# Kernel tuning notes

Hardware: AMD Instinct MI355X
Metric: run time of the kernel (lower is better)

The kernel has to match this reference:

```python
import jax, jax.numpy as jnp
import numpy as np

N, C, H, W = 4, 256, 32, 32
NH = 2                      # att_nhead
HD = C // NH                # 128 per-head dim
MAX_DIS = 7
WS = 2 * MAX_DIS + 1        # 15 window side
WW = WS * WS                # 225 window positions
T = (C / NH) ** 0.5


def _gather_idx(h, w):
    # idx[wpos, m]: flat index into zero-padded (h+14, w+14) grid of the
    # neighbor at window offset wpos for query pixel m (== F.unfold semantics)
    pw = w + 2 * MAX_DIS
    dy, dx = np.meshgrid(np.arange(WS), np.arange(WS), indexing='ij')
    ys, xs = np.meshgrid(np.arange(h), np.arange(w), indexing='ij')
    idx = (dy.reshape(-1, 1) + ys.reshape(1, -1)) * pw + (dx.reshape(-1, 1) + xs.reshape(1, -1))
    return jnp.asarray(idx, dtype=jnp.int32)  # [WW, h*w]


def setup_inputs() -> dict:
    key = jax.random.key(0)
    ks = jax.random.split(key, 14)
    s = 0.02
    return {
        'q': jax.random.normal(ks[0], (N, C, H, W), jnp.float32),
        'k': jax.random.normal(ks[1], (N, C, H, W), jnp.float32),
        'v': jax.random.normal(ks[2], (N, C, H, W), jnp.float32),
        'Wq': jax.random.normal(ks[3], (C, C), jnp.float32) * s,
        'bq': jnp.zeros((C,), jnp.float32),
        'Wk': jax.random.normal(ks[4], (C, C), jnp.float32) * s,
        'bk': jnp.zeros((C,), jnp.float32),
        'Wv': jax.random.normal(ks[5], (C, C), jnp.float32) * s,
        'bv': jnp.zeros((C,), jnp.float32),
        'Wrel': jax.random.normal(ks[6], (NH, WW, HD), jnp.float32) * s,   # grouped 1x1 conv
        'brel': jnp.zeros((NH * WW,), jnp.float32),
        'V_bias': jax.random.normal(ks[7], (NH, HD, WW), jnp.float32) * s,
        'Wfc': jax.random.normal(ks[8], (C, C), jnp.float32) * s,
        'bfc': jnp.zeros((C,), jnp.float32),
    }


def _conv1x1(x, Wt, b):
    return jnp.einsum('nchw,dc->ndhw', x, Wt) + b[None, :, None, None]


def reference(q, k, v, Wq, bq, Wk, bk, Wv, bv, Wrel, brel, V_bias, Wfc, bfc):
    n, c, h, w = q.shape
    hw = h * w
    idx = _gather_idx(h, w)                                   # [WW, hw]
    pad = ((0, 0), (0, 0), (0, 0), (MAX_DIS, MAX_DIS), (MAX_DIS, MAX_DIS))

    q = _conv1x1(q, Wq, bq)
    k = _conv1x1(k, Wk, bk)
    v = _conv1x1(v, Wv, bv)

    # grouped 1x1 conv: relative position logits, [n, NH, WW, hw]
    rel = jnp.einsum('ngcxy,gwc->ngwxy', q.reshape(n, NH, HD, h, w), Wrel)
    rel = rel + brel.reshape(NH, WW)[None, :, :, None, None]
    rel = rel.reshape(n, NH, WW, hw)

    qs = (q / T).reshape(n, NH, HD, hw)

    # unfold K via zero-pad + gather: [n, NH, HD, WW, hw]
    k_pad = jnp.pad(k.reshape(n, NH, HD, h, w), pad).reshape(n, NH, HD, -1)
    k_un = k_pad[..., idx]
    qk = jnp.einsum('ngcm,ngcwm->ngwm', qs, k_un) + rel

    # boundary mask: neighbor inside the original image
    valid = jnp.pad(jnp.ones((h, w), jnp.float32), MAX_DIS).reshape(-1)[idx] > 0
    qk = jnp.where(valid[None, None], qk, jnp.float32(-1e8))
    attn = jax.nn.softmax(qk, axis=2)                         # over window positions

    agg_bias = jnp.einsum('ngwm,gcw->mngc', attn, V_bias).reshape(hw, n, c)

    # local2global scatter + dense einsum == gather of zero-padded V
    v_pad = jnp.pad(v.reshape(n, NH, HD, h, w), pad).reshape(n, NH, HD, -1)
    v_un = v_pad[..., idx]                                    # [n, NH, HD, WW, hw]
    agg_value = jnp.einsum('ngwm,ngcwm->mngc', attn, v_un).reshape(hw, n, c)

    out = (agg_value + agg_bias) @ Wfc.T + bfc                # [hw, n, c]
    return out
```

## Files before the change

### kernel.cpp

```cpp
#include <hip/hip_runtime.h>
#include <math.h>


typedef __attribute__((ext_vector_type(8))) short short8;
typedef __attribute__((ext_vector_type(4))) short short4v;
typedef __attribute__((ext_vector_type(4))) float floatx4;

__device__ __forceinline__ short f2bf(float f) {
    unsigned u = __float_as_uint(f);
    unsigned r = (u + 0x7fffu + ((u >> 16) & 1u)) >> 16;
    return (short)r;
}
__device__ __forceinline__ float bf2f(short s) {
    return __uint_as_float(((unsigned)(unsigned short)s) << 16);
}

__global__ __launch_bounds__(256)
void conv_kernel(const float* __restrict__ q, const float* __restrict__ k,
                 const float* __restrict__ v,
                 const float* __restrict__ Wq, const float* __restrict__ Wk,
                 const float* __restrict__ Wv, const float* __restrict__ Wfc,
                 const float* __restrict__ Wrel,
                 short* __restrict__ Xhi, short* __restrict__ Xlo,
                 short* __restrict__ Whi, short* __restrict__ Wlo,
                 short* __restrict__ Wrh, short* __restrict__ Wrl)
{
    const int tid = threadIdx.x;
    const int z = blockIdx.z;
    const int lane = tid & 63;
    const int n16 = lane & 15, quad = lane >> 4;

    if (z < 12) {
        __shared__ float st[64 * 33];
        const int sel = z >> 2, batch = z & 3;
        const float* X = (sel == 0 ? q : sel == 1 ? k : v) + ((long)batch << 18);
        const int mb = blockIdx.x, kc = blockIdx.y;
#pragma unroll
        for (int it = 0; it < 8; ++it) {
            int e = tid + it * 256;
            int cc = e >> 6, mm = e & 63;
            st[mm * 33 + cc] = X[((long)(kc * 32 + cc) << 10) + mb * 64 + mm];
        }
        __syncthreads();
        const int mtl = tid >> 6;
        const int m = mtl * 16 + n16;
        short h[8], l[8];
#pragma unroll
        for (int j = 0; j < 8; ++j) {
            float f = st[m * 33 + quad * 8 + j];
            short hb = f2bf(f);
            h[j] = hb;
            l[j] = f2bf(f - bf2f(hb));
        }
        int mt16 = mb * 4 + mtl;
        long off = (long)z * 262144 + (((long)(mt16 * 8 + kc) * 64) + lane) * 8;
        *(short8*)(Xhi + off) = *(short8*)&h[0];
        *(short8*)(Xlo + off) = *(short8*)&l[0];
    } else if (z < 16) {
        if (tid >= 64) return;
        const int w = z - 12;
        const float* W = (w == 0 ? Wq : w == 1 ? Wk : w == 2 ? Wv : Wfc);
        const int dt = blockIdx.x, kc = blockIdx.y;
        const int d = dt * 16 + n16, cb = kc * 32 + quad * 8;
        float4 w0 = *(const float4*)&W[d * 256 + cb];
        float4 w1 = *(const float4*)&W[d * 256 + cb + 4];
        float f[8] = {w0.x, w0.y, w0.z, w0.w, w1.x, w1.y, w1.z, w1.w};
        short h[8], l[8];
#pragma unroll
        for (int j = 0; j < 8; ++j) {
            short hb = f2bf(f[j]);
            h[j] = hb;
            l[j] = f2bf(f[j] - bf2f(hb));
        }
        long off = (long)w * 65536 + (((long)(dt * 8 + kc) * 64) + lane) * 8;
        *(short8*)(Whi + off) = *(short8*)&h[0];
        *(short8*)(Wlo + off) = *(short8*)&l[0];
    } else {
        if (tid >= 64) return;
        const int g = z - 16;
        const int wt = blockIdx.x, kc = blockIdx.y;
        if (wt >= 15 || kc >= 4) return;
        const int w = wt * 16 + n16;
        const int cb = kc * 32 + quad * 8;
        float f[8] = {0.f, 0.f, 0.f, 0.f, 0.f, 0.f, 0.f, 0.f};
        if (w < 225) {
            float4 w0 = *(const float4*)&Wrel[(long)(g * 225 + w) * 128 + cb];
            float4 w1 = *(const float4*)&Wrel[(long)(g * 225 + w) * 128 + cb + 4];
            f[0] = w0.x; f[1] = w0.y; f[2] = w0.z; f[3] = w0.w;
            f[4] = w1.x; f[5] = w1.y; f[6] = w1.z; f[7] = w1.w;
        }
        short h[8], l[8];
#pragma unroll
        for (int j = 0; j < 8; ++j) {
            short hb = f2bf(f[j]);
            h[j] = hb;
            l[j] = f2bf(f[j] - bf2f(hb));
        }
        long off = (long)g * 30720 + (((long)(wt * 4 + kc) * 64) + lane) * 8;
        *(short8*)(Wrh + off) = *(short8*)&h[0];
        *(short8*)(Wrl + off) = *(short8*)&l[0];
    }
}

__global__ __launch_bounds__(256)
void mfma_proj(const short* __restrict__ Xhi, const short* __restrict__ Xlo,
               const short* __restrict__ Whi, const short* __restrict__ Wlo,
               const float* __restrict__ bq, const float* __restrict__ bk,
               const float* __restrict__ bv,
               short* __restrict__ qhi, short* __restrict__ qlo,
               short* __restrict__ khi, short* __restrict__ klo,
               float* __restrict__ vpad)
{
    __shared__ float tile[16 * 65];
    const int tid = threadIdx.x;
    const int wave = tid >> 6, lane = tid & 63;
    const int n16 = lane & 15, quad = lane >> 4;
    const int mt16 = blockIdx.x, db = blockIdx.y, z = blockIdx.z;
    const int sel = z >> 2, batch = z & 3;
    const int dt = db * 4 + wave;

    const short* Ah = Whi + (long)sel * 65536 + ((long)(dt * 8) * 64 + lane) * 8;
    const short* Al = Wlo + (long)sel * 65536 + ((long)(dt * 8) * 64 + lane) * 8;
    const short* Bh = Xhi + (long)z * 262144;
    const short* Bl = Xlo + (long)z * 262144;

    const float* bias = (sel == 0 ? bq : sel == 1 ? bk : bv);
    float4 bv4 = *(const float4*)&bias[dt * 16 + quad * 4];
    float bb[4] = {bv4.x, bv4.y, bv4.z, bv4.w};

    floatx4 acc = {0.f, 0.f, 0.f, 0.f};
#pragma unroll
    for (int kc = 0; kc < 8; ++kc) {
        short8 ahi = *(const short8*)(Ah + kc * 512);
        short8 alo = *(const short8*)(Al + kc * 512);
        long bo = ((long)(mt16 * 8 + kc) * 64 + lane) * 8;
        short8 bh = *(const short8*)(Bh + bo);
        short8 bl = *(const short8*)(Bl + bo);
        acc = __builtin_amdgcn_mfma_f32_16x16x32_bf16(ahi, bh, acc, 0, 0, 0);
        acc = __builtin_amdgcn_mfma_f32_16x16x32_bf16(ahi, bl, acc, 0, 0, 0);
        acc = __builtin_amdgcn_mfma_f32_16x16x32_bf16(alo, bh, acc, 0, 0, 0);
    }

    if (sel == 2) {
        const int m = mt16 * 16 + n16;
        float* Y = vpad + (long)batch * 393216;
        const int row = m >> 5, col = (m & 31) + 8;
#pragma unroll
        for (int r = 0; r < 4; ++r)
            Y[(long)(dt * 16 + quad * 4 + r) * 1536 + row * 48 + col] = acc[r] + bb[r];
        {
            const int prow = mt16 >> 1, side = mt16 & 1;
            const int ch_l = tid >> 2, f2 = (tid & 3) * 2;
            long po = (long)(db * 64 + ch_l) * 1536 + prow * 48 + side * 40 + f2;
            Y[po] = 0.f;
            Y[po + 1] = 0.f;
        }
        return;
    }

    const int cl = wave * 16 + quad * 4;
#pragma unroll
    for (int r = 0; r < 4; ++r)
        tile[n16 * 65 + cl + r] = acc[r] + bb[r];
    __syncthreads();

    const float scale = (sel == 1) ? 0.08838834764831845f : 1.0f;
    const int m_l = tid >> 4, c16 = (tid & 15) * 4;
    const int m = mt16 * 16 + m_l;
    const int cglob = db * 64 + c16;
    const int g = cglob >> 7, ch = cglob & 127;
    const long base = (((long)(batch * 2 + g) << 10) + m) * 128 + ch;
    short h[4], l[4];
#pragma unroll
    for (int j = 0; j < 4; ++j) {
        float f = tile[m_l * 65 + c16 + j] * scale;
        short hb = f2bf(f);
        h[j] = hb;
        l[j] = f2bf(f - bf2f(hb));
    }
    short* oh = sel ? khi : qhi;
    short* ol = sel ? klo : qlo;
    *(short4v*)(oh + base) = *(short4v*)&h[0];
    *(short4v*)(ol + base) = *(short4v*)&l[0];
}

__global__ __launch_bounds__(256)
void scores_mfma(const short* __restrict__ qhi, const short* __restrict__ qlo,
                 const short* __restrict__ khi, const short* __restrict__ klo,
                 const short* __restrict__ Wrh, const short* __restrict__ Wrl,
                 const float* __restrict__ brel, float* __restrict__ attn)
{
    __shared__ float qk[16 * 241];
    __shared__ float invl[16];

    const int tid = threadIdx.x;
    const int wave = tid >> 6, lane = tid & 63;
    const int y  = blockIdx.x >> 1;
    const int xt = blockIdx.x & 1;
    const int bz = blockIdx.y;
    const int g = bz & 1;
    const int x0 = xt * 16;
    float* relh = attn + (long)bz * 230400;

    const int n16 = lane & 15, quad = lane >> 4;
    const long qbase = (((long)bz << 10) + y * 32 + x0 + n16) * 128 + quad * 8;
    short8 a_hi[4], a_lo[4];
#pragma unroll
    for (int ch = 0; ch < 4; ++ch) {
        a_hi[ch] = *(const short8*)(qhi + qbase + ch * 32);
        a_lo[ch] = *(const short8*)(qlo + qbase + ch * 32);
    }

    for (int wt = wave; wt < 15; wt += 4) {
        const short* Ah = Wrh + (long)g * 30720 + ((long)(wt * 4) * 64 + lane) * 8;
        const short* Al = Wrl + (long)g * 30720 + ((long)(wt * 4) * 64 + lane) * 8;
        floatx4 racc = {0.f, 0.f, 0.f, 0.f};
#pragma unroll
        for (int kc = 0; kc < 4; ++kc) {
            short8 whh = *(const short8*)(Ah + kc * 512);
            short8 wll = *(const short8*)(Al + kc * 512);
            racc = __builtin_amdgcn_mfma_f32_16x16x32_bf16(whh, a_hi[kc], racc, 0, 0, 0);
            racc = __builtin_amdgcn_mfma_f32_16x16x32_bf16(whh, a_lo[kc], racc, 0, 0, 0);
            racc = __builtin_amdgcn_mfma_f32_16x16x32_bf16(wll, a_hi[kc], racc, 0, 0, 0);
        }
#pragma unroll
        for (int r = 0; r < 4; ++r) {
            int w = wt * 16 + quad * 4 + r;
            if (w < 225) {
                int dy = w / 15, dx = w - dy * 15;
                qk[n16 * 241 + dy * 16 + dx] = racc[r] + brel[g * 225 + w];
            }
        }
    }
    __syncthreads();

    for (int e = tid; e < 16 * 241; e += 256) {
        int px = e / 241, idx = e - px * 241;
        int dy = idx >> 4, dx = idx & 15;
        int hy = y + dy - 7, hx = x0 + px + dx - 7;
        bool valid = (dx < 15) && (dy < 15) &&
                     (hy >= 0) && (hy < 32) && (hx >= 0) && (hx < 32);
        if (!valid) qk[e] = -1e8f;
    }
    __syncthreads();

    for (int dy = wave; dy < 15; dy += 4) {
        const int ky = y + dy - 7;
        if (ky < 0 || ky > 31) continue;
#pragma unroll
        for (int kxt = 0; kxt < 2; ++kxt) {
            const int kxg = x0 - 8 + kxt * 16 + n16;
            const long kb = (((long)bz << 10) + ky * 32 + kxg) * 128 + quad * 8;
            floatx4 acc = {0.f, 0.f, 0.f, 0.f};
#pragma unroll
            for (int ch = 0; ch < 4; ++ch) {
                short8 b_hi = *(const short8*)(khi + kb + ch * 32);
                short8 b_lo = *(const short8*)(klo + kb + ch * 32);
                acc = __builtin_amdgcn_mfma_f32_16x16x32_bf16(a_hi[ch], b_hi, acc, 0, 0, 0);
                acc = __builtin_amdgcn_mfma_f32_16x16x32_bf16(a_hi[ch], b_lo, acc, 0, 0, 0);
                acc = __builtin_amdgcn_mfma_f32_16x16x32_bf16(a_lo[ch], b_hi, acc, 0, 0, 0);
            }
            if (kxg >= 0 && kxg < 32) {
#pragma unroll
                for (int r = 0; r < 4; ++r) {
                    int m = quad * 4 + r;
                    int dx = kxg - (x0 + m) + 7;
                    if (dx >= 0 && dx < 15) {
                        int s = m * 241 + dy * 16 + dx;
                        qk[s] = qk[s] + acc[r];
                    }
                }
            }
        }
    }
    __syncthreads();

    {
        int px = tid >> 4, s = tid & 15;
        float mx = -3.0e38f;
        for (int w = s; w < 240; w += 16) mx = fmaxf(mx, qk[px * 241 + w]);
#pragma unroll
        for (int msk = 8; msk; msk >>= 1) mx = fmaxf(mx, __shfl_xor(mx, msk));
        float sum = 0.f;
        for (int w = s; w < 240; w += 16) {
            float p = __expf(qk[px * 241 + w] - mx);
            qk[px * 241 + w] = p;
            sum += p;
        }
#pragma unroll
        for (int msk = 8; msk; msk >>= 1) sum += __shfl_xor(sum, msk);
        if (s == 0) invl[px] = 1.0f / sum;
    }
    __syncthreads();

    for (int e = tid; e < 3600; e += 256) {
        int px = e & 15, w = e >> 4;
        int dy2 = w / 15, dx2 = w - dy2 * 15;
        relh[((long)w << 10) + y * 32 + x0 + px] =
            qk[px * 241 + dy2 * 16 + dx2] * invl[px];
    }
}

__global__ __launch_bounds__(256)
void pv_kernel(const float* __restrict__ vpad, const float* __restrict__ attn,
               const float* __restrict__ Vbias,
               short* __restrict__ AGhi, short* __restrict__ AGlo)
{
    __shared__ __align__(16) float pa[225 * 32];
    const int tid = threadIdx.x;
    const int y   = blockIdx.x;
    const int chh = blockIdx.y;
    const int bz  = blockIdx.z;
    const int n = bz >> 1, g = bz & 1;

    const float* ab = attn + (long)bz * 230400 + y * 32;
    for (int e = tid; e < 1800; e += 256) {
        int w = e >> 3, x4 = (e & 7) * 4;
        *(float4*)&pa[w * 32 + x4] = *(const float4*)&ab[((long)w << 10) + x4];
    }
    __syncthreads();

    const int chg = tid >> 3;
    const int xq  = tid & 7;
    const int c0  = chh * 64 + chg * 2;
    const int x0  = xq * 4;
    const float* v0 = vpad + (long)bz * 196608 + (long)c0 * 1536;
    const float* v1 = v0 + 1536;
    const float* b0 = Vbias + (g * 128 + c0) * 225;
    const float* b1 = b0 + 225;

    float acc0[4] = {0.f, 0.f, 0.f, 0.f};
    float acc1[4] = {0.f, 0.f, 0.f, 0.f};

    for (int dy = 0; dy < 15; ++dy) {
        int hy = y + dy - 7;
        if (hy < 0 || hy > 31) continue;
        const float4* r0 = (const float4*)(v0 + hy * 48 + x0);
        const float4* r1 = (const float4*)(v1 + hy * 48 + x0);
        float wa[20], wb[20];
#pragma unroll
        for (int t = 0; t < 5; ++t) {
            float4 a = r0[t], b = r1[t];
            wa[4*t+0] = a.x; wa[4*t+1] = a.y; wa[4*t+2] = a.z; wa[4*t+3] = a.w;
            wb[4*t+0] = b.x; wb[4*t+1] = b.y; wb[4*t+2] = b.z; wb[4*t+3] = b.w;
        }
        const float* par = &pa[dy * 15 * 32 + x0];
        const float* vb0 = b0 + dy * 15;
        const float* vb1 = b1 + dy * 15;
#pragma unroll
        for (int dx = 0; dx < 15; ++dx) {
            float4 p4 = *(const float4*)&par[dx * 32];
            float ba = vb0[dx], bb = vb1[dx];
            acc0[0] += p4.x * (wa[1 + dx] + ba);
            acc0[1] += p4.y * (wa[2 + dx] + ba);
            acc0[2] += p4.z * (wa[3 + dx] + ba);
            acc0[3] += p4.w * (wa[4 + dx] + ba);
            acc1[0] += p4.x * (wb[1 + dx] + bb);
            acc1[1] += p4.y * (wb[2 + dx] + bb);
            acc1[2] += p4.z * (wb[3 + dx] + bb);
            acc1[3] += p4.w * (wb[4 + dx] + bb);
        }
    }
    __syncthreads();

    float* tile = pa;
#pragma unroll
    for (int i = 0; i < 4; ++i) {
        tile[(x0 + i) * 65 + chg * 2 + 0] = acc0[i];
        tile[(x0 + i) * 65 + chg * 2 + 1] = acc1[i];
    }
    __syncthreads();

    const int lane = tid & 63, sub = tid >> 6;
    const int kcp = sub & 1, mtp = sub >> 1;
    const int n16 = lane & 15, quad = lane >> 4;
    const int m_loc = mtp * 16 + n16;
    const int c_loc = kcp * 32 + quad * 8;
    short h[8], l[8];
#pragma unroll
    for (int j = 0; j < 8; ++j) {
        float f = tile[m_loc * 65 + c_loc + j];
        short hb = f2bf(f);
        h[j] = hb;
        l[j] = f2bf(f - bf2f(hb));
    }
    const int mt16 = y * 2 + mtp;
    const int kc = g * 4 + chh * 2 + kcp;
    long off = (long)n * 262144 + (((long)(mt16 * 8 + kc) * 64) + lane) * 8;
    *(short8*)(AGhi + off) = *(short8*)&h[0];
    *(short8*)(AGlo + off) = *(short8*)&l[0];
}

__global__ __launch_bounds__(256)
void mfma_fc(const short* __restrict__ Ahi, const short* __restrict__ Alo,
             const short* __restrict__ Whi, const short* __restrict__ Wlo,
             const float* __restrict__ bfc, float* __restrict__ out)
{
    __shared__ float tile[16 * 68];
    const int tid = threadIdx.x;
    const int wave = tid >> 6, lane = tid & 63;
    const int n16 = lane & 15, quad = lane >> 4;
    const int mt16 = blockIdx.x, db = blockIdx.y, nz = blockIdx.z;
    const int dt = db * 4 + wave;

    const short* Ah = Whi + (long)3 * 65536 + ((long)(dt * 8) * 64 + lane) * 8;
    const short* Al = Wlo + (long)3 * 65536 + ((long)(dt * 8) * 64 + lane) * 8;
    const short* Bh = Ahi + (long)nz * 262144;
    const short* Bl = Alo + (long)nz * 262144;

    float4 bv4 = *(const float4*)&bfc[dt * 16 + quad * 4];
    float bb[4] = {bv4.x, bv4.y, bv4.z, bv4.w};

    floatx4 acc = {0.f, 0.f, 0.f, 0.f};
#pragma unroll
    for (int kc = 0; kc < 8; ++kc) {
        short8 ahi = *(const short8*)(Ah + kc * 512);
        short8 alo = *(const short8*)(Al + kc * 512);
        long bo = ((long)(mt16 * 8 + kc) * 64 + lane) * 8;
        short8 bh = *(const short8*)(Bh + bo);
        short8 bl = *(const short8*)(Bl + bo);
        acc = __builtin_amdgcn_mfma_f32_16x16x32_bf16(ahi, bh, acc, 0, 0, 0);
        acc = __builtin_amdgcn_mfma_f32_16x16x32_bf16(ahi, bl, acc, 0, 0, 0);
        acc = __builtin_amdgcn_mfma_f32_16x16x32_bf16(alo, bh, acc, 0, 0, 0);
    }

    const int dl = wave * 16 + quad * 4;
#pragma unroll
    for (int r = 0; r < 4; ++r)
        tile[n16 * 68 + dl + r] = acc[r] + bb[r];
    __syncthreads();

    const int mm = tid >> 4, d4 = (tid & 15) * 4;
    float4 o4 = *(const float4*)&tile[mm * 68 + d4];
    *(float4*)&out[(long)(mt16 * 16 + mm) * 1024 + nz * 256 + db * 64 + d4] = o4;
}

extern "C" void kernel_launch(void* const* d_in, const int* in_sizes, int n_in,
                              void* d_out, int out_size, void* d_ws, size_t ws_size,
                              hipStream_t stream)
{
    const float* q    = (const float*)d_in[0];
    const float* k    = (const float*)d_in[1];
    const float* v    = (const float*)d_in[2];
    const float* Wq   = (const float*)d_in[3];
    const float* bq   = (const float*)d_in[4];
    const float* Wk   = (const float*)d_in[5];
    const float* bk   = (const float*)d_in[6];
    const float* Wv   = (const float*)d_in[7];
    const float* bv   = (const float*)d_in[8];
    const float* Wrel = (const float*)d_in[9];
    const float* brel = (const float*)d_in[10];
    const float* Vb   = (const float*)d_in[11];
    const float* Wfc  = (const float*)d_in[12];
    const float* bfc  = (const float*)d_in[13];
    float* out = (float*)d_out;

    float* ws   = (float*)d_ws;
    float* vpad = ws + 2097152;
    float* attn = ws + 4718592;
    short* qhi  = (short*)(ws + 6561792);
    short* qlo  = (short*)(ws + 7086080);
    short* khi  = (short*)(ws + 7610368);
    short* klo  = (short*)(ws + 8134656);
    short* Xhi  = (short*)(ws + 8658944);
    short* Xlo  = (short*)(ws + 10231808);
    short* Whi  = (short*)(ws + 11804672);
    short* Wlo  = (short*)(ws + 11935744);
    short* AGhi = (short*)(ws + 12066816);
    short* AGlo = (short*)(ws + 12591104);
    short* Wrh  = (short*)(ws + 13115392);
    short* Wrl  = (short*)(ws + 13146112);

    dim3 blk(256);

    conv_kernel<<<dim3(16, 8, 18), blk, 0, stream>>>(q, k, v, Wq, Wk, Wv, Wfc,
                                                     Wrel, Xhi, Xlo, Whi, Wlo,
                                                     Wrh, Wrl);

    mfma_proj<<<dim3(64, 4, 12), blk, 0, stream>>>(Xhi, Xlo, Whi, Wlo,
                                                   bq, bk, bv,
                                                   qhi, qlo, khi, klo, vpad);

    scores_mfma<<<dim3(64, 8), blk, 0, stream>>>(qhi, qlo, khi, klo,
                                                 Wrh, Wrl, brel, attn);

    pv_kernel<<<dim3(32, 2, 8), blk, 0, stream>>>(vpad, attn, Vb, AGhi, AGlo);

    mfma_fc<<<dim3(64, 4, 4), blk, 0, stream>>>(AGhi, AGlo, Whi, Wlo, bfc, out);
}
```

Measured before the change: 169.0 us.

## Fuse attention scores/softmax with PV aggregation into one kernel

Merges the scores kernel and the PV kernel so softmax probabilities stay in shared memory instead of being written to and re-read from a global attention buffer. Each block now handles 16 pixels and all 128 channels of its head, which changes the thread mapping for PV and the AG output tile layout. This removes one launch and the global round trip of the attention matrix. In exchange it uses more shared memory per block and gives fewer, heavier blocks (512 vs the previous separate grids), which may lower occupancy.

```diff
diff --git a/kernel.cpp b/kernel.cpp
--- a/kernel.cpp
+++ b/kernel.cpp
@@ -185,12 +185,16 @@
 }
 
 __global__ __launch_bounds__(256)
-void scores_mfma(const short* __restrict__ qhi, const short* __restrict__ qlo,
-                 const short* __restrict__ khi, const short* __restrict__ klo,
-                 const short* __restrict__ Wrh, const short* __restrict__ Wrl,
-                 const float* __restrict__ brel, float* __restrict__ attn)
+void scores_pv(const short* __restrict__ qhi, const short* __restrict__ qlo,
+               const short* __restrict__ khi, const short* __restrict__ klo,
+               const short* __restrict__ Wrh, const short* __restrict__ Wrl,
+               const float* __restrict__ brel,
+               const float* __restrict__ vpad, const float* __restrict__ Vbias,
+               short* __restrict__ AGhi, short* __restrict__ AGlo)
 {
     __shared__ float qk[16 * 241];
+    __shared__ float pa2[225 * 16];
+    __shared__ float tile[16 * 133];
     __shared__ float invl[16];
 
     const int tid = threadIdx.x;
@@ -200,7 +204,6 @@
     const int bz = blockIdx.y;
     const int g = bz & 1;
     const int x0 = xt * 16;
-    float* relh = attn + (long)bz * 230400;
 
     const int n16 = lane & 15, quad = lane >> 4;
     const long qbase = (((long)bz << 10) + y * 32 + x0 + n16) * 128 + quad * 8;
@@ -294,36 +297,17 @@
     __syncthreads();
 
     for (int e = tid; e < 3600; e += 256) {
-        int px = e & 15, w = e >> 4;
+        int w = e >> 4, px = e & 15;
         int dy2 = w / 15, dx2 = w - dy2 * 15;
-        relh[((long)w << 10) + y * 32 + x0 + px] =
-            qk[px * 241 + dy2 * 16 + dx2] * invl[px];
-    }
-}
-
-__global__ __launch_bounds__(256)
-void pv_kernel(const float* __restrict__ vpad, const float* __restrict__ attn,
-               const float* __restrict__ Vbias,
-               short* __restrict__ AGhi, short* __restrict__ AGlo)
-{
-    __shared__ __align__(16) float pa[225 * 32];
-    const int tid = threadIdx.x;
-    const int y   = blockIdx.x;
-    const int chh = blockIdx.y;
-    const int bz  = blockIdx.z;
-    const int n = bz >> 1, g = bz & 1;
-
-    const float* ab = attn + (long)bz * 230400 + y * 32;
-    for (int e = tid; e < 1800; e += 256) {
-        int w = e >> 3, x4 = (e & 7) * 4;
-        *(float4*)&pa[w * 32 + x4] = *(const float4*)&ab[((long)w << 10) + x4];
-    }
-    __syncthreads();
-
-    const int chg = tid >> 3;
-    const int xq  = tid & 7;
-    const int c0  = chh * 64 + chg * 2;
-    const int x0  = xq * 4;
+        pa2[w * 16 + px] = qk[px * 241 + dy2 * 16 + dx2] * invl[px];
+    }
+    __syncthreads();
+
+    const int n = bz >> 1;
+    const int chg2 = tid >> 2;
+    const int xq   = tid & 3;
+    const int c0   = chg2 * 2;
+    const int xb   = x0 + xq * 4;
     const float* v0 = vpad + (long)bz * 196608 + (long)c0 * 1536;
     const float* v1 = v0 + 1536;
     const float* b0 = Vbias + (g * 128 + c0) * 225;
@@ -335,8 +319,8 @@
     for (int dy = 0; dy < 15; ++dy) {
         int hy = y + dy - 7;
         if (hy < 0 || hy > 31) continue;
-        const float4* r0 = (const float4*)(v0 + hy * 48 + x0);
-        const float4* r1 = (const float4*)(v1 + hy * 48 + x0);
+        const float4* r0 = (const float4*)(v0 + hy * 48 + xb);
+        const float4* r1 = (const float4*)(v1 + hy * 48 + xb);
         float wa[20], wb[20];
 #pragma unroll
         for (int t = 0; t < 5; ++t) {
@@ -344,12 +328,12 @@
             wa[4*t+0] = a.x; wa[4*t+1] = a.y; wa[4*t+2] = a.z; wa[4*t+3] = a.w;
             wb[4*t+0] = b.x; wb[4*t+1] = b.y; wb[4*t+2] = b.z; wb[4*t+3] = b.w;
         }
-        const float* par = &pa[dy * 15 * 32 + x0];
+        const float* par = &pa2[dy * 15 * 16 + xq * 4];
         const float* vb0 = b0 + dy * 15;
         const float* vb1 = b1 + dy * 15;
 #pragma unroll
         for (int dx = 0; dx < 15; ++dx) {
-            float4 p4 = *(const float4*)&par[dx * 32];
+            float4 p4 = *(const float4*)&par[dx * 16];
             float ba = vb0[dx], bb = vb1[dx];
             acc0[0] += p4.x * (wa[1 + dx] + ba);
             acc0[1] += p4.y * (wa[2 + dx] + ba);
@@ -361,31 +345,25 @@
             acc1[3] += p4.w * (wb[4 + dx] + bb);
         }
     }
-    __syncthreads();
-
-    float* tile = pa;
+
 #pragma unroll
     for (int i = 0; i < 4; ++i) {
-        tile[(x0 + i) * 65 + chg * 2 + 0] = acc0[i];
-        tile[(x0 + i) * 65 + chg * 2 + 1] = acc1[i];
-    }
-    __syncthreads();
-
-    const int lane = tid & 63, sub = tid >> 6;
-    const int kcp = sub & 1, mtp = sub >> 1;
-    const int n16 = lane & 15, quad = lane >> 4;
-    const int m_loc = mtp * 16 + n16;
-    const int c_loc = kcp * 32 + quad * 8;
+        tile[(xq * 4 + i) * 133 + c0 + 0] = acc0[i];
+        tile[(xq * 4 + i) * 133 + c0 + 1] = acc1[i];
+    }
+    __syncthreads();
+
+    const int sub = tid >> 6;
     short h[8], l[8];
 #pragma unroll
     for (int j = 0; j < 8; ++j) {
-        float f = tile[m_loc * 65 + c_loc + j];
+        float f = tile[n16 * 133 + sub * 32 + quad * 8 + j];
         short hb = f2bf(f);
         h[j] = hb;
         l[j] = f2bf(f - bf2f(hb));
     }
-    const int mt16 = y * 2 + mtp;
-    const int kc = g * 4 + chh * 2 + kcp;
+    const int mt16 = y * 2 + xt;
+    const int kc = g * 4 + sub;
     long off = (long)n * 262144 + (((long)(mt16 * 8 + kc) * 64) + lane) * 8;
     *(short8*)(AGhi + off) = *(short8*)&h[0];
     *(short8*)(AGlo + off) = *(short8*)&l[0];
@@ -457,7 +435,6 @@
 
     float* ws   = (float*)d_ws;
     float* vpad = ws + 2097152;
-    float* attn = ws + 4718592;
     short* qhi  = (short*)(ws + 6561792);
     short* qlo  = (short*)(ws + 7086080);
     short* khi  = (short*)(ws + 7610368);
@@ -481,10 +458,9 @@
                                                    bq, bk, bv,
                                                    qhi, qlo, khi, klo, vpad);
 
-    scores_mfma<<<dim3(64, 8), blk, 0, stream>>>(qhi, qlo, khi, klo,
-                                                 Wrh, Wrl, brel, attn);
-
-    pv_kernel<<<dim3(32, 2, 8), blk, 0, stream>>>(vpad, attn, Vb, AGhi, AGlo);
+    scores_pv<<<dim3(64, 8), blk, 0, stream>>>(qhi, qlo, khi, klo,
+                                               Wrh, Wrl, brel,
+                                               vpad, Vb, AGhi, AGlo);
 
     mfma_fc<<<dim3(64, 4, 4), blk, 0, stream>>>(AGhi, AGlo, Whi, Wlo, bfc, out);
 }
```

Result: no change. 169.9 us (+0.5%).
